# Kernel tuning notes

Measured on AMD Instinct MI355X. Metric: run time of the kernel, lower is better.

The kernel has to match this reference:

```python
import jax, jax.numpy as jnp
import numpy as np
import math

B, T, C_EMB, H, M, P = 4, 8192, 1024, 16, 64, 8
D = C_EMB // H
L = int(math.log2(T // M)) - 1  # = 6 levels of coarse attention
SCALE_ATTN = True
NEG = -1e30


def setup_inputs() -> dict:
    key = jax.random.key(0)
    ks = jax.random.split(key, 4)
    x = jax.random.normal(ks[0], (B, T, C_EMB), jnp.float32)
    W_attn = jax.random.normal(ks[1], (C_EMB, 3 * C_EMB), jnp.float32) * (1.0 / math.sqrt(C_EMB))
    b_attn = jnp.zeros((3 * C_EMB,), jnp.float32)
    W_proj = jax.random.normal(ks[2], (C_EMB, C_EMB), jnp.float32) * (1.0 / math.sqrt(C_EMB))
    b_proj = jnp.zeros((C_EMB,), jnp.float32)
    return {"x": x, "W_attn": W_attn, "b_attn": b_attn, "W_proj": W_proj, "b_proj": b_proj}


def _shift(t, s):
    # shift blocks forward along axis 1 by s, zero-padding at the front
    pad = jnp.zeros_like(t[:, :s])
    return jnp.concatenate([pad, t[:, :-s]], axis=1)


def _fma_attention(q, k, v):
    # q, k, v: [BH, T, D]; q already scaled by 1/sqrt(D)
    BH = q.shape[0]
    # --- convolute(): avgpool downsampled K, V at each level ---
    Kls, Vls = [k], [v]
    for l in range(L):
        r = (M * 2 ** l) // P  # pool kernel = stride
        Kls.append(k.reshape(BH, T // r, r, D).mean(axis=2))
        Vls.append(v.reshape(BH, T // r, r, D).mean(axis=2))
    # --- stage1: banded QK at every level ---
    As = []
    # fine level 0: causal sliding window of M keys (j in [i-M+1, i])
    nb0 = T // M
    qb = q.reshape(BH, nb0, M, D)
    kb = k.reshape(BH, nb0, M, D)
    s_prev = jnp.einsum('bgqd,bgkd->bgqk', qb, _shift(kb, 1))
    s_self = jnp.einsum('bgqd,bgkd->bgqk', qb, kb)
    r_idx = jnp.arange(M)[:, None]
    c_idx = jnp.arange(M)[None, :]
    g_ok = (jnp.arange(nb0) >= 1)[None, :, None, None]
    s_prev = jnp.where((c_idx > r_idx) & g_ok, s_prev, NEG)
    s_self = jnp.where(c_idx <= r_idx, s_self, NEG)
    As.append(jnp.concatenate([s_prev, s_self], axis=-1).reshape(BH, T, 2 * M))
    # coarse levels l=1..L: query block (width w) attends to the P summaries of
    # each of the two preceding coarse blocks (causal, left-to-right)
    for l in range(1, L + 1):
        w = M * 2 ** (l - 1)
        nb = T // w
        qw = q.reshape(BH, nb, w, D)
        kc = Kls[l].reshape(BH, nb, P, D)
        scores = []
        for s in (2, 1):
            sc = jnp.einsum('bgqd,bgpd->bgqp', qw, _shift(kc, s))
            ok = (jnp.arange(nb) >= s)[None, :, None, None]
            scores.append(jnp.where(ok, sc, NEG))
        As.append(jnp.concatenate(scores, axis=-1).reshape(BH, T, 2 * P))
    # --- fused multi-level softmax (shared max + shared normalizer) ---
    gmax = jnp.max(jnp.stack([a.max(axis=-1) for a in As], axis=-1), axis=-1)  # [BH, T]
    Es = [jnp.exp(a - gmax[..., None]) for a in As]
    scales = [1] + [((M * 2 ** (l - 1)) // P if SCALE_ATTN else 1) for l in range(1, L + 1)]
    denom = sum(float(s) * e.sum(axis=-1) for s, e in zip(scales, Es))[..., None]
    Cs = [float(s) * e / denom for s, e in zip(scales, Es)]
    # --- stage2: banded CV ---
    vb = v.reshape(BH, nb0, M, D)
    C0 = Cs[0].reshape(BH, nb0, M, 2 * M)
    out = (jnp.einsum('bgqk,bgkd->bgqd', C0[..., :M], _shift(vb, 1)) +
           jnp.einsum('bgqk,bgkd->bgqd', C0[..., M:], vb)).reshape(BH, T, D)
    for l in range(1, L + 1):
        w = M * 2 ** (l - 1)
        nb = T // w
        vc = Vls[l].reshape(BH, nb, P, D)
        Cl = Cs[l].reshape(BH, nb, w, 2 * P)
        ol = (jnp.einsum('bgqp,bgpd->bgqd', Cl[..., :P], _shift(vc, 2)) +
              jnp.einsum('bgqp,bgpd->bgqd', Cl[..., P:], _shift(vc, 1)))
        out = out + ol.reshape(BH, T, D)
    return out


def reference(x, W_attn, b_attn, W_proj, b_proj):
    Bx, Tx, Cx = x.shape
    qkv = x @ W_attn + b_attn
    q, k, v = jnp.split(qkv, 3, axis=-1)

    def heads(t):
        return t.reshape(Bx, Tx, H, D).transpose(0, 2, 1, 3).reshape(Bx * H, Tx, D)

    q = heads(q) / math.sqrt(D)
    o = _fma_attention(q, heads(k), heads(v))
    o = o.reshape(Bx, H, Tx, D).transpose(0, 2, 1, 3).reshape(Bx, Tx, Cx)
    return o @ W_proj + b_proj
```

## Files before the change

### kernel.cpp

```cpp
#include <hip/hip_runtime.h>
#include <hip/hip_bf16.h>
#include <stdint.h>


typedef float  f32x4  __attribute__((ext_vector_type(4)));
typedef __bf16 bf16x8 __attribute__((ext_vector_type(8)));
typedef unsigned short ushort8 __attribute__((ext_vector_type(8)));
typedef unsigned short ushort4v __attribute__((ext_vector_type(4)));

__device__ __forceinline__ unsigned short f2bf(float f) {
  union { float f; unsigned u; } v; v.f = f;
  unsigned r = v.u + 0x7fffu + ((v.u >> 16) & 1u);
  return (unsigned short)(r >> 16);
}
__device__ __forceinline__ float bf2f(unsigned short s) {
  union { unsigned u; float f; } v; v.u = ((unsigned)s) << 16;
  return v.f;
}
__device__ __forceinline__ bf16x8 ld_bf8(const unsigned short* p) {
  return __builtin_bit_cast(bf16x8, *(const ushort8*)p);
}
__device__ __forceinline__ f32x4 mfma16(bf16x8 a, bf16x8 b, f32x4 c) {
  return __builtin_amdgcn_mfma_f32_16x16x32_bf16(a, b, c, 0, 0, 0);
}
__device__ __forceinline__ f32x4 zero4() {
  f32x4 z; z[0] = 0.f; z[1] = 0.f; z[2] = 0.f; z[3] = 0.f; return z;
}
__device__ __forceinline__ void gload16(const void* g, void* lds) {
  __builtin_amdgcn_global_load_lds(
      (const __attribute__((address_space(1))) void*)(uintptr_t)g,
      (__attribute__((address_space(3))) void*)(unsigned int)(uintptr_t)lds,
      16, 0, 0);
}

#define T_SEQ 8192
#define NPOOL 2016

__global__ __launch_bounds__(256) void castx_k(const float* __restrict__ x,
                                               unsigned short* __restrict__ xb) {
  size_t i = ((size_t)blockIdx.x * 256 + threadIdx.x) * 8;
  float4 a = *(const float4*)(x + i);
  float4 b = *(const float4*)(x + i + 4);
  ushort8 o;
  o[0] = f2bf(a.x); o[1] = f2bf(a.y); o[2] = f2bf(a.z); o[3] = f2bf(a.w);
  o[4] = f2bf(b.x); o[5] = f2bf(b.y); o[6] = f2bf(b.z); o[7] = f2bf(b.w);
  *(ushort8*)(xb + i) = o;
}

__global__ __launch_bounds__(256) void transposeW_k(const float* __restrict__ w,
                                                    unsigned short* __restrict__ wt,
                                                    int R, int C) {
  __shared__ float tile[64 * 65];
  int cc = blockIdx.x, rc = blockIdx.y;
  int tid = threadIdx.x;
#pragma unroll
  for (int p = 0; p < 4; ++p) {
    int ci = p * 256 + tid;
    int r = ci >> 4, q4 = ci & 15;
    float4 v = *(const float4*)(w + (size_t)(rc * 64 + r) * C + cc * 64 + q4 * 4);
    tile[r * 65 + q4 * 4 + 0] = v.x;
    tile[r * 65 + q4 * 4 + 1] = v.y;
    tile[r * 65 + q4 * 4 + 2] = v.z;
    tile[r * 65 + q4 * 4 + 3] = v.w;
  }
  __syncthreads();
#pragma unroll
  for (int p = 0; p < 2; ++p) {
    int orow = p * 32 + (tid >> 3), tg = tid & 7;
    ushort8 ov;
#pragma unroll
    for (int i = 0; i < 8; ++i) ov[i] = f2bf(tile[(tg * 8 + i) * 65 + orow]);
    *(ushort8*)(wt + (size_t)(cc * 64 + orow) * R + rc * 64 + tg * 8) = ov;
  }
}

template<int NTILE_N, int EPI>
__global__ __launch_bounds__(512, 2) void gemm256(
    const unsigned short* __restrict__ A, const unsigned short* __restrict__ Bt,
    const float* __restrict__ bias,
    unsigned short* __restrict__ o0, unsigned short* __restrict__ o1,
    unsigned short* __restrict__ o2, float* __restrict__ fout) {
  extern __shared__ __align__(16) char smem[];
  const int K = 1024;
  const int nwg = 128 * NTILE_N;
  const int q = nwg >> 3;
  const int wg = ((int)blockIdx.x & 7) * q + ((int)blockIdx.x >> 3);
  const int tm = wg & 127, tn = wg >> 7;
  const int tid = threadIdx.x;
  const int wid = tid >> 6, lane = tid & 63;
  const int wm = wid >> 2, wn = wid & 3;
  const int lr = lane & 15, lg = lane >> 4;

  const int srow = tid >> 2;
  const int sseg = (tid & 3) ^ ((tid >> 3) & 3);
  const unsigned short* aSrc = A + (size_t)(tm * 256 + srow) * K + sseg * 8;
  const unsigned short* bSrc = Bt + (size_t)(tn * 256 + srow) * K + sseg * 8;
  const unsigned ldsT = (unsigned)tid * 16;

  const unsigned psel = (unsigned)((lg ^ ((lr >> 1) & 3)) * 16);
  const unsigned aBase = (unsigned)(wm * 8192 + lr * 64) + psel;
  const unsigned bBase = (unsigned)(16384 + wn * 4096 + lr * 64) + psel;

  f32x4 acc[8][4];
#pragma unroll
  for (int i = 0; i < 8; ++i)
#pragma unroll
    for (int j = 0; j < 4; ++j) acc[i][j] = zero4();

  bf16x8 rA0[4], rA1[4], rB0[4], rB1[4];

  auto SB = [&]() {
    __builtin_amdgcn_sched_barrier(0);
    __builtin_amdgcn_s_barrier();
    __builtin_amdgcn_sched_barrier(0);
  };
  auto VM4 = [&]() {
    __builtin_amdgcn_sched_barrier(0);
    asm volatile("s_waitcnt vmcnt(4)" ::: "memory");
    __builtin_amdgcn_sched_barrier(0);
  };
  auto VM0 = [&]() {
    __builtin_amdgcn_sched_barrier(0);
    asm volatile("s_waitcnt vmcnt(0)" ::: "memory");
    __builtin_amdgcn_sched_barrier(0);
  };
  auto stage2 = [&](int coffShorts, unsigned slotB) {
#pragma unroll
    for (int pass = 0; pass < 2; ++pass) {
      gload16(aSrc + (size_t)pass * 128 * K + coffShorts,
              smem + slotB + pass * 8192 + ldsT);
      gload16(bSrc + (size_t)pass * 128 * K + coffShorts,
              smem + slotB + 16384 + pass * 8192 + ldsT);
    }
  };
  auto rdA = [&](bf16x8 (&dst)[4], unsigned slotB, int ih) {
    const char* p = smem + slotB + aBase + ih * 4096;
#pragma unroll
    for (int ii = 0; ii < 4; ++ii)
      dst[ii] = ld_bf8((const unsigned short*)(p + ii * 1024));
  };
  auto rdB = [&](bf16x8 (&dst)[4], unsigned slotB) {
    const char* p = smem + slotB + bBase;
#pragma unroll
    for (int j = 0; j < 4; ++j)
      dst[j] = ld_bf8((const unsigned short*)(p + j * 1024));
  };
  auto cluster = [&](int rb, bf16x8 (&a)[4], bf16x8 (&b)[4]) {
    __builtin_amdgcn_s_setprio(1);
#pragma unroll
    for (int ii = 0; ii < 4; ++ii)
#pragma unroll
      for (int j = 0; j < 4; ++j)
        acc[rb + ii][j] = mfma16(b[j], a[ii], acc[rb + ii][j]);
    __builtin_amdgcn_s_setprio(0);
  };

  auto steady = [&](int t, unsigned s0B, unsigned s1B, unsigned sn0B,
                    unsigned sn1B) {
    const int cn = (t + 1) * 64;
    stage2(cn, sn0B);
    rdA(rA1, s0B, 1);
    VM4();
    SB();
    cluster(0, rA0, rB0);
    stage2(cn + 32, sn1B);
    rdA(rA0, s1B, 0);
    rdB(rB1, s1B);
    SB();
    cluster(4, rA1, rB0);
    rdA(rA1, s1B, 1);
    VM4();
    SB();
    cluster(0, rA0, rB1);
    rdA(rA0, sn0B, 0);
    rdB(rB0, sn0B);
    SB();
    cluster(4, rA1, rB1);
  };

  stage2(0, 0u);
  stage2(32, 32768u);
  VM4();
  SB();
  rdA(rA0, 0u, 0);
  rdB(rB0, 0u);

  for (int tp = 0; tp < 7; ++tp) {
    steady(2 * tp, 0u, 32768u, 65536u, 98304u);
    steady(2 * tp + 1, 65536u, 98304u, 0u, 32768u);
  }
  steady(14, 0u, 32768u, 65536u, 98304u);

  rdA(rA1, 65536u, 1);
  VM0();
  SB();
  cluster(0, rA0, rB0);
  rdA(rA0, 98304u, 0);
  rdB(rB1, 98304u);
  SB();
  cluster(4, rA1, rB0);
  rdA(rA1, 98304u, 1);
  SB();
  cluster(0, rA0, rB1);
  SB();
  cluster(4, rA1, rB1);

  const int mBase = tm * 256 + wm * 128;
  const int nBase = tn * 256 + wn * 64;
  if (EPI == 0) {
    const int region = nBase >> 10, nn = nBase & 1023, hh = nn >> 6;
    unsigned short* dst = region == 0 ? o0 : (region == 1 ? o1 : o2);
#pragma unroll
    for (int j = 0; j < 4; ++j) {
      const int d0 = (nn & 63) + j * 16 + lg * 4;
      const float4 bv = *(const float4*)(bias + nBase + j * 16 + lg * 4);
#pragma unroll
      for (int i = 0; i < 8; ++i) {
        const int m = mBase + i * 16 + lr;
        const int bb = m >> 13, tq = m & 8191;
        ushort4v pk;
        pk[0] = f2bf(acc[i][j][0] + bv.x);
        pk[1] = f2bf(acc[i][j][1] + bv.y);
        pk[2] = f2bf(acc[i][j][2] + bv.z);
        pk[3] = f2bf(acc[i][j][3] + bv.w);
        *(ushort4v*)(dst + (((size_t)(bb * 16 + hh)) * T_SEQ + tq) * 64 + d0) = pk;
      }
    }
  } else {
#pragma unroll
    for (int j = 0; j < 4; ++j) {
      const int n0 = nBase + j * 16 + lg * 4;
      const float4 bv = *(const float4*)(bias + n0);
#pragma unroll
      for (int i = 0; i < 8; ++i) {
        const int m = mBase + i * 16 + lr;
        float4 ov;
        ov.x = acc[i][j][0] + bv.x;
        ov.y = acc[i][j][1] + bv.y;
        ov.z = acc[i][j][2] + bv.z;
        ov.w = acc[i][j][3] + bv.w;
        *(float4*)(fout + (size_t)m * 1024 + n0) = ov;
      }
    }
  }
}

__global__ __launch_bounds__(256) void transposeV_k(const unsigned short* __restrict__ v,
                                                    unsigned short* __restrict__ vt) {
  __shared__ float tile[64 * 65];
  int tc = blockIdx.x, bh = blockIdx.y;
  int tid = threadIdx.x;
#pragma unroll
  for (int p = 0; p < 2; ++p) {
    int r = p * 32 + (tid >> 3), cg = tid & 7;
    ushort8 u = *(const ushort8*)(v + ((size_t)bh * T_SEQ + (size_t)tc * 64 + r) * 64 + cg * 8);
#pragma unroll
    for (int i = 0; i < 8; ++i) tile[r * 65 + cg * 8 + i] = bf2f(u[i]);
  }
  __syncthreads();
#pragma unroll
  for (int p = 0; p < 2; ++p) {
    int dd = p * 32 + (tid >> 3), tg = tid & 7;
    ushort8 ov;
#pragma unroll
    for (int i = 0; i < 8; ++i) ov[i] = f2bf(tile[(tg * 8 + i) * 65 + dd]);
    *(ushort8*)(vt + ((size_t)bh * 64 + dd) * T_SEQ + (size_t)tc * 64 + tg * 8) = ov;
  }
}

__global__ __launch_bounds__(256) void poolK_k(const unsigned short* __restrict__ kin,
                                               unsigned short* __restrict__ kpool) {
  __shared__ float buf[64 * 65];
  int chunk = blockIdx.x, bh = blockIdx.y;
  int tid = threadIdx.x;
  int cg = tid & 7, orow = tid >> 3;
  float s[8];
#pragma unroll
  for (int i = 0; i < 8; ++i) s[i] = 0.f;
  const unsigned short* base =
      kin + ((size_t)bh * T_SEQ + chunk * 256 + orow * 8) * 64 + cg * 8;
#pragma unroll
  for (int rr = 0; rr < 8; ++rr) {
    ushort8 v = *(const ushort8*)(base + (size_t)rr * 64);
#pragma unroll
    for (int i = 0; i < 8; ++i) s[i] += bf2f(v[i]);
  }
  unsigned short* kp = kpool + (size_t)bh * NPOOL * 64;
  {
    ushort8 ov;
#pragma unroll
    for (int i = 0; i < 8; ++i) {
      s[i] *= 0.125f;
      ov[i] = f2bf(s[i]);
      buf[orow * 65 + cg * 8 + i] = s[i];
    }
    *(ushort8*)(kp + ((size_t)(chunk * 32 + orow)) * 64 + cg * 8) = ov;
  }
  __syncthreads();
  int srcR = 0, dstR = 32;
#pragma unroll
  for (int lvl = 2; lvl <= 6; ++lvl) {
    int rows = 32 >> (lvl - 1);
    int off = 2048 - (2048 >> (lvl - 1));
    if (orow < rows) {
      ushort8 ov;
      float tv[8];
#pragma unroll
      for (int i = 0; i < 8; ++i) {
        tv[i] = 0.5f * (buf[(srcR + 2 * orow) * 65 + cg * 8 + i] +
                        buf[(srcR + 2 * orow + 1) * 65 + cg * 8 + i]);
        ov[i] = f2bf(tv[i]);
      }
      *(ushort8*)(kp + ((size_t)(off + chunk * rows + orow)) * 64 + cg * 8) = ov;
#pragma unroll
      for (int i = 0; i < 8; ++i) buf[(dstR + orow) * 65 + cg * 8 + i] = tv[i];
    }
    __syncthreads();
    srcR = dstR;
    dstR += rows;
  }
}

__global__ __launch_bounds__(256) void poolV_k(const unsigned short* __restrict__ vt,
                                               unsigned short* __restrict__ vtpool) {
  __shared__ float buf[1024 + 512 + 256 + 128 + 64];
  int d = blockIdx.x, bh = blockIdx.y;
  int tid = threadIdx.x;
  const unsigned short* src = vt + ((size_t)bh * 64 + d) * T_SEQ;
  unsigned short* dst = vtpool + ((size_t)bh * 64 + d) * NPOOL;
#pragma unroll
  for (int p = 0; p < 4; ++p) {
    int oi = p * 256 + tid;
    ushort8 v = *(const ushort8*)(src + (size_t)oi * 8);
    float s = 0.f;
#pragma unroll
    for (int i = 0; i < 8; ++i) s += bf2f(v[i]);
    s *= 0.125f;
    dst[oi] = f2bf(s);
    buf[oi] = s;
  }
  __syncthreads();
  float* b1 = buf; float* b2 = buf + 1024;
#pragma unroll
  for (int p = 0; p < 2; ++p) {
    int oi = p * 256 + tid;
    float s = 0.5f * (b1[2 * oi] + b1[2 * oi + 1]);
    dst[1024 + oi] = f2bf(s);
    b2[oi] = s;
  }
  __syncthreads();
  float* b3 = b2 + 512;
  {
    float s = 0.5f * (b2[2 * tid] + b2[2 * tid + 1]);
    dst[1536 + tid] = f2bf(s);
    b3[tid] = s;
  }
  __syncthreads();
  float* b4 = b3 + 256;
  if (tid < 128) {
    float s = 0.5f * (b3[2 * tid] + b3[2 * tid + 1]);
    dst[1792 + tid] = f2bf(s);
    b4[tid] = s;
  }
  __syncthreads();
  float* b5 = b4 + 128;
  if (tid < 64) {
    float s = 0.5f * (b4[2 * tid] + b4[2 * tid + 1]);
    dst[1920 + tid] = f2bf(s);
    b5[tid] = s;
  }
  __syncthreads();
  if (tid < 32) {
    float s = 0.5f * (b5[2 * tid] + b5[2 * tid + 1]);
    dst[1984 + tid] = f2bf(s);
  }
}

__global__ __launch_bounds__(256) void attn_k(const unsigned short* __restrict__ q,
                                              const unsigned short* __restrict__ k,
                                              const unsigned short* __restrict__ kpool,
                                              const unsigned short* __restrict__ vt,
                                              const unsigned short* __restrict__ vtpool,
                                              unsigned short* __restrict__ o) {
  const int g = blockIdx.x;
  const int bh = blockIdx.y;
  const int tid = threadIdx.x;
  const int w = tid >> 6, l = tid & 63;
  const int lr = l & 15, lg = l >> 4;
  __shared__ unsigned short KV[224 * 64];
  __shared__ unsigned short Pl[64 * 264];

  const size_t qoff = ((size_t)bh * T_SEQ + (size_t)g * 64 + w * 16 + lr) * 64 + lg * 8;
  bf16x8 aq0 = ld_bf8(q + qoff);
  bf16x8 aq1 = ld_bf8(q + qoff + 32);
  __builtin_amdgcn_sched_barrier(0);

  const int krow = tid >> 3;
  const int kseg = tid & 7;
#pragma unroll
  for (int p = 0; p < 7; ++p) {
    const int row = p * 32 + krow;
    const unsigned short* src;
    if (row < 128) {
      int t0 = (g - 1) * 64 + row;
      if (t0 < 0) t0 = 0;
      src = k + ((size_t)bh * T_SEQ + t0) * 64;
    } else {
      const int pr = row - 128;
      const int lvl0 = pr >> 4;
      const int off = 2048 - (2048 >> lvl0);
      const int gl = g >> lvl0;
      int st = (gl - 2) * 8 + (pr & 15);
      if (st < 0) st = 0;
      src = kpool + ((size_t)bh * NPOOL + off + st) * 64;
    }
    gload16(src + (kseg ^ (row & 7)) * 8,
            ((char*)KV) + p * 4096 + (unsigned)tid * 16);
  }
  __builtin_amdgcn_sched_barrier(0);

  const int vr = tid >> 2;
  const int vg = tid & 3;
  const int vswz = vg ^ ((vr >> 1) & 3);
  ushort8 vstg[7];
#pragma unroll
  for (int s = 0; s < 7; ++s) {
    const int colsh = s * 32 + vswz * 8;
    const unsigned short* src;
    if (colsh < 128) {
      int t0 = (g - 1) * 64 + colsh;
      if (t0 < 0) t0 = 0;
      src = vt + ((size_t)bh * 64 + vr) * T_SEQ + t0;
    } else {
      const int c = colsh - 128;
      const int lvl = c >> 4;
      const int off = 2048 - (2048 >> lvl);
      const int gl = g >> lvl;
      int start = (gl - 2) * 8 + (c & 15);
      if (start < 0) start = 0;
      src = vtpool + ((size_t)bh * 64 + vr) * NPOOL + off + start;
    }
    vstg[s] = *(const ushort8*)src;
  }
  __builtin_amdgcn_sched_barrier(0);
  asm volatile("s_waitcnt vmcnt(7)" ::: "memory");
  __builtin_amdgcn_sched_barrier(0);
  __builtin_amdgcn_s_barrier();
  __builtin_amdgcn_sched_barrier(0);

  f32x4 S[14];
#pragma unroll
  for (int ct = 0; ct < 14; ++ct) S[ct] = zero4();
#pragma unroll
  for (int ct = 0; ct < 14; ++ct) {
    const int row = ct * 16 + lr;
    const unsigned short* kr = KV + row * 64;
    const int sw = row & 7;
    S[ct] = mfma16(aq0, ld_bf8(kr + (lg ^ sw) * 8), S[ct]);
    S[ct] = mfma16(aq1, ld_bf8(kr + ((lg + 4) ^ sw) * 8), S[ct]);
  }
  __builtin_amdgcn_sched_barrier(0);
  __builtin_amdgcn_s_barrier();
  __builtin_amdgcn_sched_barrier(0);

  const float NEGF = -1e30f;
#pragma unroll
  for (int ct = 0; ct < 14; ++ct) {
#pragma unroll
    for (int e = 0; e < 4; ++e) {
      int rr = w * 16 + lg * 4 + e;
      float s = S[ct][e] * 0.125f;
      bool valid;
      if (ct < 8) {
        int cc = ct * 16 + lr;
        valid = (cc > rr) && (cc <= rr + 64) && ((g >= 1) || (cc >= 64));
      } else {
        int lvl = ct - 7;
        int gl = g >> (lvl - 1);
        valid = gl >= ((lr < 8) ? 2 : 1);
      }
      S[ct][e] = valid ? s : NEGF;
    }
  }
  float mrow[4], invd[4];
#pragma unroll
  for (int e = 0; e < 4; ++e) {
    float mx = S[0][e];
#pragma unroll
    for (int ct = 1; ct < 14; ++ct) mx = fmaxf(mx, S[ct][e]);
    mx = fmaxf(mx, __shfl_xor(mx, 1));
    mx = fmaxf(mx, __shfl_xor(mx, 2));
    mx = fmaxf(mx, __shfl_xor(mx, 4));
    mx = fmaxf(mx, __shfl_xor(mx, 8));
    mrow[e] = mx;
  }
#pragma unroll
  for (int e = 0; e < 4; ++e) {
    float sum = 0.f;
#pragma unroll
    for (int ct = 0; ct < 14; ++ct) {
      float sc = (ct < 8) ? 1.0f : (float)(8 << (ct - 8));
      float ev = sc * __expf(S[ct][e] - mrow[e]);
      S[ct][e] = ev;
      sum += ev;
    }
    sum += __shfl_xor(sum, 1);
    sum += __shfl_xor(sum, 2);
    sum += __shfl_xor(sum, 4);
    sum += __shfl_xor(sum, 8);
    invd[e] = 1.0f / sum;
  }
#pragma unroll
  for (int ct = 0; ct < 14; ++ct) {
#pragma unroll
    for (int e = 0; e < 4; ++e) {
      int rr = w * 16 + lg * 4 + e;
      Pl[rr * 264 + ct * 16 + lr] = f2bf(S[ct][e] * invd[e]);
    }
  }
#pragma unroll
  for (int s = 0; s < 7; ++s)
    *(ushort8*)&KV[s * 2048 + vr * 32 + vg * 8] = vstg[s];
  __syncthreads();

  f32x4 O[4];
#pragma unroll
  for (int c2 = 0; c2 < 4; ++c2) O[c2] = zero4();
#pragma unroll
  for (int kc = 0; kc < 7; ++kc) {
    bf16x8 pa = ld_bf8(&Pl[(w * 16 + lr) * 264 + kc * 32 + lg * 8]);
#pragma unroll
    for (int c2 = 0; c2 < 4; ++c2) {
      const int row = c2 * 16 + lr;
      bf16x8 vb = ld_bf8(&KV[kc * 2048 + row * 32 + ((lg ^ ((lr >> 1) & 3)) * 8)]);
      O[c2] = mfma16(pa, vb, O[c2]);
    }
  }
  const int bb = bh >> 4, hh = bh & 15;
#pragma unroll
  for (int c2 = 0; c2 < 4; ++c2) {
    int d = c2 * 16 + lr;
#pragma unroll
    for (int e = 0; e < 4; ++e) {
      int t = g * 64 + w * 16 + lg * 4 + e;
      o[((size_t)bb * T_SEQ + t) * 1024 + hh * 64 + d] = f2bf(O[c2][e]);
    }
  }
}

extern "C" void kernel_launch(void* const* d_in, const int* in_sizes, int n_in,
                              void* d_out, int out_size, void* d_ws, size_t ws_size,
                              hipStream_t stream) {
  const float* x  = (const float*)d_in[0];
  const float* Wa = (const float*)d_in[1];
  const float* ba = (const float*)d_in[2];
  const float* Wp = (const float*)d_in[3];
  const float* bp = (const float*)d_in[4];
  float* out = (float*)d_out;
  char* ws = (char*)d_ws;
  const size_t MB = 1024 * 1024;

  unsigned short* xb  = (unsigned short*)(ws);
  unsigned short* qb  = (unsigned short*)(ws + 64 * MB);
  unsigned short* kb  = (unsigned short*)(ws + 128 * MB);
  unsigned short* vb  = (unsigned short*)(ws + 192 * MB);
  unsigned short* vt  = (unsigned short*)(ws + 256 * MB);
  unsigned short* wat = (unsigned short*)(ws + 320 * MB);
  unsigned short* wpt = (unsigned short*)(ws + 326 * MB);
  unsigned short* kpool  = xb;
  unsigned short* vtpool = (unsigned short*)(ws + 32 * MB);

  hipFuncSetAttribute((const void*)gemm256<12, 0>,
                      hipFuncAttributeMaxDynamicSharedMemorySize, 131072);
  hipFuncSetAttribute((const void*)gemm256<4, 1>,
                      hipFuncAttributeMaxDynamicSharedMemorySize, 131072);

  castx_k<<<16384, 256, 0, stream>>>(x, xb);
  transposeW_k<<<dim3(48, 16), 256, 0, stream>>>(Wa, wat, 1024, 3072);
  transposeW_k<<<dim3(16, 16), 256, 0, stream>>>(Wp, wpt, 1024, 1024);
  gemm256<12, 0><<<1536, 512, 131072, stream>>>(xb, wat, ba, qb, kb, vb, nullptr);
  transposeV_k<<<dim3(128, 64), 256, 0, stream>>>(vb, vt);
  poolK_k<<<dim3(32, 64), 256, 0, stream>>>(kb, kpool);
  poolV_k<<<dim3(64, 64), 256, 0, stream>>>(vt, vtpool);
  attn_k<<<dim3(128, 64), 256, 0, stream>>>(qb, kb, kpool, vt, vtpool, vb);
  gemm256<4, 1><<<512, 512, 131072, stream>>>(vb, wpt, bp, nullptr, nullptr, nullptr, out);
}
```

Measured before the change: 547.7 us.

## Deepen GEMM LDS pipeline to four-slot prefetch with two half-tiles in flight

The bf16 GEMM main loop used a double-buffered scheme: each k-step issued the global-to-LDS loads for the next 64-wide k-chunk and waited with vmcnt(4). It now primes all four 32 KB LDS slots up front and, inside a unified 16-iteration loop, issues the load for chunk t+2 into the slot just consumed. The wait counts rise to vmcnt(8), so roughly two chunks of global loads stay in flight during the MFMA clusters, hiding more memory latency. In exchange the loop control and tail waits are more complex, and the slot reuse ordering must stay correct against the barriers.

After: 536.7 us. 1.02x faster.

```diff
diff --git a/kernel.cpp b/kernel.cpp
--- a/kernel.cpp
+++ b/kernel.cpp
@@ -35,6 +35,14 @@
 
 #define T_SEQ 8192
 #define NPOOL 2016
+
+#define SCHED0() __builtin_amdgcn_sched_barrier(0)
+#define VMC(n)                                           \
+  do {                                                   \
+    SCHED0();                                            \
+    asm volatile("s_waitcnt vmcnt(" #n ")" ::: "memory");\
+    SCHED0();                                            \
+  } while (0)
 
 __global__ __launch_bounds__(256) void castx_k(const float* __restrict__ x,
                                                unsigned short* __restrict__ xb) {
@@ -110,19 +118,9 @@
   bf16x8 rA0[4], rA1[4], rB0[4], rB1[4];
 
   auto SB = [&]() {
-    __builtin_amdgcn_sched_barrier(0);
+    SCHED0();
     __builtin_amdgcn_s_barrier();
-    __builtin_amdgcn_sched_barrier(0);
-  };
-  auto VM4 = [&]() {
-    __builtin_amdgcn_sched_barrier(0);
-    asm volatile("s_waitcnt vmcnt(4)" ::: "memory");
-    __builtin_amdgcn_sched_barrier(0);
-  };
-  auto VM0 = [&]() {
-    __builtin_amdgcn_sched_barrier(0);
-    asm volatile("s_waitcnt vmcnt(0)" ::: "memory");
-    __builtin_amdgcn_sched_barrier(0);
+    SCHED0();
   };
   auto stage2 = [&](int coffShorts, unsigned slotB) {
 #pragma unroll
@@ -155,55 +153,37 @@
     __builtin_amdgcn_s_setprio(0);
   };
 
-  auto steady = [&](int t, unsigned s0B, unsigned s1B, unsigned sn0B,
-                    unsigned sn1B) {
-    const int cn = (t + 1) * 64;
-    stage2(cn, sn0B);
-    rdA(rA1, s0B, 1);
-    VM4();
-    SB();
-    cluster(0, rA0, rB0);
-    stage2(cn + 32, sn1B);
-    rdA(rA0, s1B, 0);
-    rdB(rB1, s1B);
-    SB();
-    cluster(4, rA1, rB0);
-    rdA(rA1, s1B, 1);
-    VM4();
-    SB();
-    cluster(0, rA0, rB1);
-    rdA(rA0, sn0B, 0);
-    rdB(rB0, sn0B);
-    SB();
-    cluster(4, rA1, rB1);
-  };
-
   stage2(0, 0u);
   stage2(32, 32768u);
-  VM4();
+  stage2(64, 65536u);
+  stage2(96, 98304u);
+  VMC(12);
   SB();
   rdA(rA0, 0u, 0);
   rdB(rB0, 0u);
 
-  for (int tp = 0; tp < 7; ++tp) {
-    steady(2 * tp, 0u, 32768u, 65536u, 98304u);
-    steady(2 * tp + 1, 65536u, 98304u, 0u, 32768u);
-  }
-  steady(14, 0u, 32768u, 65536u, 98304u);
-
-  rdA(rA1, 65536u, 1);
-  VM0();
-  SB();
-  cluster(0, rA0, rB0);
-  rdA(rA0, 98304u, 0);
-  rdB(rB1, 98304u);
-  SB();
-  cluster(4, rA1, rB0);
-  rdA(rA1, 98304u, 1);
-  SB();
-  cluster(0, rA0, rB1);
-  SB();
-  cluster(4, rA1, rB1);
+  for (int t = 0; t < 16; ++t) {
+    const unsigned s0  = (unsigned)((2 * t) & 3) * 32768u;
+    const unsigned s1  = (unsigned)((2 * t + 1) & 3) * 32768u;
+    const unsigned sn0 = (unsigned)((2 * t + 2) & 3) * 32768u;
+    rdA(rA1, s0, 1);
+    if (t < 15) { VMC(8); } else { VMC(0); }
+    SB();
+    cluster(0, rA0, rB0);
+    if (t < 14) stage2((t + 2) * 64, s0);
+    rdA(rA0, s1, 0);
+    rdB(rB1, s1);
+    SB();
+    cluster(4, rA1, rB0);
+    rdA(rA1, s1, 1);
+    if (t < 14) { VMC(8); } else if (t == 14) { VMC(4); }
+    SB();
+    cluster(0, rA0, rB1);
+    if (t < 14) stage2((t + 2) * 64 + 32, s1);
+    if (t < 15) { rdA(rA0, sn0, 0); rdB(rB0, sn0); }
+    SB();
+    cluster(4, rA1, rB1);
+  }
 
   const int mBase = tm * 256 + wm * 128;
   const int nBase = tn * 256 + wn * 64;
@@ -393,7 +373,7 @@
   const size_t qoff = ((size_t)bh * T_SEQ + (size_t)g * 64 + w * 16 + lr) * 64 + lg * 8;
   bf16x8 aq0 = ld_bf8(q + qoff);
   bf16x8 aq1 = ld_bf8(q + qoff + 32);
-  __builtin_amdgcn_sched_barrier(0);
+  SCHED0();
 
   const int krow = tid >> 3;
   const int kseg = tid & 7;
@@ -417,7 +397,7 @@
     gload16(src + (kseg ^ (row & 7)) * 8,
             ((char*)KV) + p * 4096 + (unsigned)tid * 16);
   }
-  __builtin_amdgcn_sched_barrier(0);
+  SCHED0();
 
   const int vr = tid >> 2;
   const int vg = tid & 3;
@@ -442,11 +422,11 @@
     }
     vstg[s] = *(const ushort8*)src;
   }
-  __builtin_amdgcn_sched_barrier(0);
+  SCHED0();
   asm volatile("s_waitcnt vmcnt(7)" ::: "memory");
-  __builtin_amdgcn_sched_barrier(0);
+  SCHED0();
   __builtin_amdgcn_s_barrier();
-  __builtin_amdgcn_sched_barrier(0);
+  SCHED0();
 
   f32x4 S[14];
 #pragma unroll
@@ -459,9 +439,9 @@
     S[ct] = mfma16(aq0, ld_bf8(kr + (lg ^ sw) * 8), S[ct]);
     S[ct] = mfma16(aq1, ld_bf8(kr + ((lg + 4) ^ sw) * 8), S[ct]);
   }
-  __builtin_amdgcn_sched_barrier(0);
+  SCHED0();
   __builtin_amdgcn_s_barrier();
-  __builtin_amdgcn_sched_barrier(0);
+  SCHED0();
 
   const float NEGF = -1e30f;
 #pragma unroll
```
